# Kernel optimization log

Measured on AMD Instinct MI355X. Metric: run time of the kernel, lower is better.

The kernel has to match this reference:

```python
import jax, jax.numpy as jnp
import numpy as np

B, CIN, G, H, HW, WMIX = 128, 64, 8, 14, 16, 16  # batch, in-ch, groups, spatial, mixed width


def setup_inputs() -> dict:
    key = jax.random.key(0)
    k1, k2, k3 = jax.random.split(key, 3)
    x = jax.random.normal(k1, (B, CIN, G, H, H), dtype=jnp.float32)
    w_conv = jax.random.normal(k2, (G, 3, 3, 32), dtype=jnp.float32)   # weights[0]
    w_mix = jax.random.normal(k3, (CIN, WMIX), dtype=jnp.float32)       # weights[1]
    return {"x": x, "w_conv": w_conv, "w_mix": w_mix}


def _unfold3(t, axis, size):
    # torch F.unfold with kernel (3,1), padding (1,0) along `axis`: zero-pad by 1
    # and stack the 3 shifted windows as a new axis inserted at `axis`.
    pad = [(0, 0)] * t.ndim
    pad[axis] = (1, 1)
    p = jnp.pad(t, pad)
    slices = []
    for k in range(3):
        idx = [slice(None)] * t.ndim
        idx[axis] = slice(k, k + size)
        slices.append(p[tuple(idx)])
    return jnp.stack(slices, axis=axis)


def reference(x, w_conv, w_mix):
    # channel mix: (B, 64, 8, 14, 14) x (64, 16) -> (B, 8, 14, 14, 16)
    t4 = jnp.einsum('kjmnl,ji->kmnli', x, w_mix)
    # first unfold along H (axis 3): (B, 8, 14, 3, 14, 16)
    u1 = _unfold3(t4, 3, H)
    # second unfold along H (now axis 4): (B, 8, 14, 3, 3, 14, 16)
    u2 = _unfold3(u1, 4, H)
    # permute (0,1,2,5,4,3,6) -> (B, 8, 14, 14, 3, 3, 16)
    t5 = jnp.transpose(u2, (0, 1, 2, 5, 4, 3, 6))
    # conv channel mix: contract group(8) and both 3-taps -> (B, 14, 14, 16, 32)
    t6 = jnp.einsum('mlonikp,likj->monpj', t5, w_conv)
    # (B, 14, 14, 32, 16) -> (B, 14, 14, 512)
    t7 = jnp.transpose(t6, (0, 1, 2, 4, 3)).reshape(B, H, H, 512)
    t7 = jnp.roll(t7, 1, axis=1)  # shift_direction fixed to +1
    return jnp.transpose(t7, (0, 3, 1, 2))  # (B, 512, 14, 14)
```

## Files before the change

### kernel.cpp

```cpp
#include <hip/hip_runtime.h>

static constexpr int NB   = 128;
static constexpr int NCIN = 64;
static constexpr int NG   = 8;
static constexpr int NH   = 14;
static constexpr int NP   = 16;
static constexpr int HH   = NH * NH;
static constexpr int LROW = 20;

static constexpr int OFF_T4 = 0;
static constexpr int OFF_W2 = 2560;
static constexpr int OFF_WC = 3840;
static constexpr int OFF_XS = 2560;
static constexpr int LDS_FLOATS = 7680;

__global__ __launch_bounds__(256, 5) void fused_kernel(const float* __restrict__ x,
                                                       const float* __restrict__ wconv,
                                                       const float* __restrict__ wmix,
                                                       float* __restrict__ out) {
    __shared__ __align__(16) float lds[LDS_FLOATS];
    float*  t4s = lds + OFF_T4;
    float*  w2s = lds + OFF_W2;
    float*  wcs = lds + OFF_WC;
    float4* xs4 = reinterpret_cast<float4*>(lds + OFF_XS);

    const int tid   = threadIdx.x;
    const int b     = blockIdx.x / NH;
    const int o     = blockIdx.x % NH;
    const int o_src = (o + NH - 1) % NH;

    const float* xb = x + (size_t)b * (NCIN * NG * HH) + o_src * NH;

    const int  lane128 = tid & 127;
    const bool xact    = lane128 < 112;
    const int  jrow    = tid >> 7;
    const int  gS      = lane128 / 14;
    const int  lS      = lane128 % 14;
    const int  glst    = lane128 + (lane128 >> 3);

    float xr[16];
    const float* xb0 = xb + (size_t)(jrow * 16) * (NG * HH) + gS * HH + lS;
    if (xact) {
#pragma unroll
        for (int r = 0; r < 16; r++) xr[r] = xb0[(size_t)r * (NG * HH)];
    }

    const int gW = tid >> 5, jW = tid & 31;
    float wv9[9];
    {
        const float* wp = wconv + (size_t)(gW * 9) * 32 + jW;
#pragma unroll
        for (int t = 0; t < 9; t++) wv9[t] = wp[t * 32];
    }

#pragma unroll
    for (int r = 0; r < 3; r++) {
        int idx = r * 256 + tid;
        int gp  = idx / 6;
        int s   = idx % 6;
        int l2  = (s < 2) ? s : (14 + s);
        t4s[gp * LROW + l2] = 0.f;
    }

    if (xact) {
        float* xw = lds + OFF_XS + (jrow * 4 * 126 + glst) * 4;
#pragma unroll
        for (int r = 0; r < 16; r++)
            xw[(r >> 2) * (126 * 4) + (r & 3)] = xr[r];
    }
    __syncthreads();

    if (xact) {
        const float* xb1 = xb0 + (size_t)32 * (NG * HH);
#pragma unroll
        for (int r = 0; r < 16; r++) xr[r] = xb1[(size_t)r * (NG * HH)];
    }

    const int p0 = __builtin_amdgcn_readfirstlane((tid >> 7) << 3);
    float am[8] = {0.f, 0.f, 0.f, 0.f, 0.f, 0.f, 0.f, 0.f};

    if (xact) {
#pragma unroll
        for (int j4 = 0; j4 < 8; j4++) {
            float4 xq = xs4[j4 * 126 + glst];
#pragma unroll
            for (int pp = 0; pp < 8; pp++) {
                const int p = p0 + pp;
                am[pp] += xq.x * wmix[(j4 * 4 + 0) * NP + p]
                        + xq.y * wmix[(j4 * 4 + 1) * NP + p]
                        + xq.z * wmix[(j4 * 4 + 2) * NP + p]
                        + xq.w * wmix[(j4 * 4 + 3) * NP + p];
            }
        }
    }
    __syncthreads();
    if (xact) {
        float* xw = lds + OFF_XS + (jrow * 4 * 126 + glst) * 4;
#pragma unroll
        for (int r = 0; r < 16; r++)
            xw[(r >> 2) * (126 * 4) + (r & 3)] = xr[r];
    }
    __syncthreads();

    if (xact) {
        const float* wm1 = wmix + 32 * NP;
#pragma unroll
        for (int j4 = 0; j4 < 8; j4++) {
            float4 xq = xs4[j4 * 126 + glst];
#pragma unroll
            for (int pp = 0; pp < 8; pp++) {
                const int p = p0 + pp;
                am[pp] += xq.x * wm1[(j4 * 4 + 0) * NP + p]
                        + xq.y * wm1[(j4 * 4 + 1) * NP + p]
                        + xq.z * wm1[(j4 * 4 + 2) * NP + p]
                        + xq.w * wm1[(j4 * 4 + 3) * NP + p];
            }
        }
#pragma unroll
        for (int pp = 0; pp < 8; pp++) {
            t4s[(gS * 16 + p0 + pp) * LROW + lS + 2] = am[pp];
        }
    }
    __syncthreads();

    {
        float d0 = wv9[0];
        float d1 = wv9[1] + wv9[3];
        float d2 = wv9[2] + wv9[4] + wv9[6];
        float d3 = wv9[5] + wv9[7];
        float d4 = wv9[8];
        float* wp2 = w2s + gW * 160 + jW;
        wp2[0]   = d0;
        wp2[32]  = d1;
        wp2[64]  = d2;
        wp2[96]  = d3;
        wp2[128] = d4;
        wcs[gW * 32 + jW]       = wv9[2];
        wcs[256 + gW * 32 + jW] = wv9[6];
    }
    __syncthreads();

    const int p  = tid & 15;
    const int jh = tid >> 4;
    const int jb = jh * 2;

    float acc[NH][2];
#pragma unroll
    for (int n = 0; n < NH; n++) { acc[n][0] = 0.f; acc[n][1] = 0.f; }

    for (int g = 0; g < NG; g++) {
        float row[LROW];
        const float* rp = &t4s[(g * 16 + p) * LROW];
#pragma unroll
        for (int q = 0; q < 5; q++) {
            float4 v = *reinterpret_cast<const float4*>(rp + q * 4);
            row[q * 4 + 0] = v.x; row[q * 4 + 1] = v.y;
            row[q * 4 + 2] = v.z; row[q * 4 + 3] = v.w;
        }
#pragma unroll
        for (int di = 0; di < 5; di++) {
            float2 w = *reinterpret_cast<const float2*>(&w2s[(g * 5 + di) * 32 + jb]);
#pragma unroll
            for (int n = 0; n < NH; n++) {
                float rv = row[n + di];
                acc[n][0] += rv * w.x;
                acc[n][1] += rv * w.y;
            }
        }
        float2 c0 = *reinterpret_cast<const float2*>(&wcs[g * 32 + jb]);
        float2 c1 = *reinterpret_cast<const float2*>(&wcs[256 + g * 32 + jb]);
        float r2 = row[2], r15 = row[15];
        acc[0][0]  -= r2  * c0.x; acc[0][1]  -= r2  * c0.y;
        acc[13][0] -= r15 * c1.x; acc[13][1] -= r15 * c1.y;
    }

    __syncthreads();

    {
        int rotw = jh * 2;
        rotw -= (rotw >= 14) ? 14 : 0;
        rotw -= (rotw >= 14) ? 14 : 0;
#pragma unroll
        for (int jj = 0; jj < 2; jj++) {
            int sb = ((jb + jj) * 16 + p) * 15;
#pragma unroll
            for (int n = 0; n < NH; n++) {
                int rn = n + rotw;
                rn -= (rn >= 14) ? 14 : 0;
                lds[sb + rn] = acc[n][jj];
            }
        }
    }
    __syncthreads();

    {
        const int  k7   = tid & 7;
        const bool kact = k7 < 7;
        const int  cb   = tid >> 3;
        float* ob = out + (size_t)b * 512 * HH + (size_t)o * NH;
        if (kact) {
#pragma unroll
            for (int r = 0; r < 16; r++) {
                int c   = cb + 32 * r;
                int rot = (2 * r) % 14;
                int rn  = 2 * k7 + rot;
                rn -= (rn >= 14) ? 14 : 0;
                float v0 = lds[c * 15 + rn];
                float v1 = lds[c * 15 + rn + 1];
                *reinterpret_cast<float2*>(ob + (size_t)c * HH + 2 * k7) =
                    make_float2(v0, v1);
            }
        }
    }
}

extern "C" void kernel_launch(void* const* d_in, const int* in_sizes, int n_in,
                              void* d_out, int out_size, void* d_ws, size_t ws_size,
                              hipStream_t stream) {
    const float* x     = (const float*)d_in[0];
    const float* wconv = (const float*)d_in[1];
    const float* wmix  = (const float*)d_in[2];
    float* out = (float*)d_out;
    (void)d_ws; (void)ws_size;

    fused_kernel<<<NB * NH, 256, 0, stream>>>(x, wconv, wmix, out);
}
```

Baseline: 131.7 us.

## Drop LDS x staging, register double-buffer loads, split output transpose to cut LDS

Removes the LDS staging of x for the channel mix. Each thread now loads its 64 input channels straight from global into two 16-element register buffers, interleaving loads with FMAs. The output transpose is split into two halves so the LDS footprint shrinks (7680 to 4352 floats), and launch bounds rise to 8 blocks per CU for more occupancy. The trade-off is more register pressure, extra barriers in the store phase, and uncoalesced strided global loads replacing the shared-memory exchange.

```diff
diff --git a/kernel.cpp b/kernel.cpp
--- a/kernel.cpp
+++ b/kernel.cpp
@@ -11,39 +11,36 @@
 static constexpr int OFF_T4 = 0;
 static constexpr int OFF_W2 = 2560;
 static constexpr int OFF_WC = 3840;
-static constexpr int OFF_XS = 2560;
-static constexpr int LDS_FLOATS = 7680;
+static constexpr int LDS_FLOATS = 4352;
 
-__global__ __launch_bounds__(256, 5) void fused_kernel(const float* __restrict__ x,
+#define FMAQ(buf, qb)                                                          \
+    do {                                                                       \
+        _Pragma("unroll")                                                      \
+        for (int j4 = 0; j4 < 4; j4++) {                                       \
+            _Pragma("unroll")                                                  \
+            for (int pp = 0; pp < 8; pp++) {                                   \
+                const int p_ = p0 + pp;            \
+                am[pp] += buf[j4 * 4 + 0] * wmix[((qb) + j4 * 4 + 0) * NP + p_]\
+                        + buf[j4 * 4 + 1] * wmix[((qb) + j4 * 4 + 1) * NP + p_]\
+                        + buf[j4 * 4 + 2] * wmix[((qb) + j4 * 4 + 2) * NP + p_]\
+                        + buf[j4 * 4 + 3] * wmix[((qb) + j4 * 4 + 3) * NP + p_];\
+            }                                                                  \
+        }                                                                      \
+    } while (0)
+
+__global__ __launch_bounds__(256, 8) void fused_kernel(const float* __restrict__ x,
                                                        const float* __restrict__ wconv,
                                                        const float* __restrict__ wmix,
                                                        float* __restrict__ out) {
     __shared__ __align__(16) float lds[LDS_FLOATS];
-    float*  t4s = lds + OFF_T4;
-    float*  w2s = lds + OFF_W2;
-    float*  wcs = lds + OFF_WC;
-    float4* xs4 = reinterpret_cast<float4*>(lds + OFF_XS);
+    float* t4s = lds + OFF_T4;
+    float* w2s = lds + OFF_W2;
+    float* wcs = lds + OFF_WC;
 
     const int tid   = threadIdx.x;
     const int b     = blockIdx.x / NH;
     const int o     = blockIdx.x % NH;
     const int o_src = (o + NH - 1) % NH;
-
-    const float* xb = x + (size_t)b * (NCIN * NG * HH) + o_src * NH;
-
-    const int  lane128 = tid & 127;
-    const bool xact    = lane128 < 112;
-    const int  jrow    = tid >> 7;
-    const int  gS      = lane128 / 14;
-    const int  lS      = lane128 % 14;
-    const int  glst    = lane128 + (lane128 >> 3);
-
-    float xr[16];
-    const float* xb0 = xb + (size_t)(jrow * 16) * (NG * HH) + gS * HH + lS;
-    if (xact) {
-#pragma unroll
-        for (int r = 0; r < 16; r++) xr[r] = xb0[(size_t)r * (NG * HH)];
-    }
 
     const int gW = tid >> 5, jW = tid & 31;
     float wv9[9];
@@ -53,75 +50,19 @@
         for (int t = 0; t < 9; t++) wv9[t] = wp[t * 32];
     }
 
-#pragma unroll
-    for (int r = 0; r < 3; r++) {
-        int idx = r * 256 + tid;
-        int gp  = idx / 6;
-        int s   = idx % 6;
-        int l2  = (s < 2) ? s : (14 + s);
-        t4s[gp * LROW + l2] = 0.f;
-    }
+    const int  lane128 = tid & 127;
+    const bool xact    = lane128 < 112;
+    const int  gS      = lane128 / 14;
+    const int  lS      = lane128 % 14;
+    const int  p0      = __builtin_amdgcn_readfirstlane((tid >> 7) << 3);
+    const float* xg    = x + (size_t)b * (NCIN * NG * HH) + (size_t)gS * HH
+                           + o_src * NH + lS;
 
-    if (xact) {
-        float* xw = lds + OFF_XS + (jrow * 4 * 126 + glst) * 4;
-#pragma unroll
-        for (int r = 0; r < 16; r++)
-            xw[(r >> 2) * (126 * 4) + (r & 3)] = xr[r];
-    }
-    __syncthreads();
-
-    if (xact) {
-        const float* xb1 = xb0 + (size_t)32 * (NG * HH);
-#pragma unroll
-        for (int r = 0; r < 16; r++) xr[r] = xb1[(size_t)r * (NG * HH)];
-    }
-
-    const int p0 = __builtin_amdgcn_readfirstlane((tid >> 7) << 3);
-    float am[8] = {0.f, 0.f, 0.f, 0.f, 0.f, 0.f, 0.f, 0.f};
-
+    float xq0[16], xq1[16];
     if (xact) {
 #pragma unroll
-        for (int j4 = 0; j4 < 8; j4++) {
-            float4 xq = xs4[j4 * 126 + glst];
-#pragma unroll
-            for (int pp = 0; pp < 8; pp++) {
-                const int p = p0 + pp;
-                am[pp] += xq.x * wmix[(j4 * 4 + 0) * NP + p]
-                        + xq.y * wmix[(j4 * 4 + 1) * NP + p]
-                        + xq.z * wmix[(j4 * 4 + 2) * NP + p]
-                        + xq.w * wmix[(j4 * 4 + 3) * NP + p];
-            }
-        }
+        for (int r = 0; r < 16; r++) xq0[r] = xg[(size_t)r * (NG * HH)];
     }
-    __syncthreads();
-    if (xact) {
-        float* xw = lds + OFF_XS + (jrow * 4 * 126 + glst) * 4;
-#pragma unroll
-        for (int r = 0; r < 16; r++)
-            xw[(r >> 2) * (126 * 4) + (r & 3)] = xr[r];
-    }
-    __syncthreads();
-
-    if (xact) {
-        const float* wm1 = wmix + 32 * NP;
-#pragma unroll
-        for (int j4 = 0; j4 < 8; j4++) {
-            float4 xq = xs4[j4 * 126 + glst];
-#pragma unroll
-            for (int pp = 0; pp < 8; pp++) {
-                const int p = p0 + pp;
-                am[pp] += xq.x * wm1[(j4 * 4 + 0) * NP + p]
-                        + xq.y * wm1[(j4 * 4 + 1) * NP + p]
-                        + xq.z * wm1[(j4 * 4 + 2) * NP + p]
-                        + xq.w * wm1[(j4 * 4 + 3) * NP + p];
-            }
-        }
-#pragma unroll
-        for (int pp = 0; pp < 8; pp++) {
-            t4s[(gS * 16 + p0 + pp) * LROW + lS + 2] = am[pp];
-        }
-    }
-    __syncthreads();
 
     {
         float d0 = wv9[0];
@@ -137,6 +78,32 @@
         wp2[128] = d4;
         wcs[gW * 32 + jW]       = wv9[2];
         wcs[256 + gW * 32 + jW] = wv9[6];
+    }
+#pragma unroll
+    for (int r = 0; r < 3; r++) {
+        int idx = r * 256 + tid;
+        int gp  = idx / 6;
+        int s   = idx % 6;
+        int l2  = (s < 2) ? s : (14 + s);
+        t4s[gp * LROW + l2] = 0.f;
+    }
+
+    float am[8] = {0.f, 0.f, 0.f, 0.f, 0.f, 0.f, 0.f, 0.f};
+    if (xact) {
+#pragma unroll
+        for (int r = 0; r < 16; r++) xq1[r] = xg[(size_t)(16 + r) * (NG * HH)];
+        FMAQ(xq0, 0);
+#pragma unroll
+        for (int r = 0; r < 16; r++) xq0[r] = xg[(size_t)(32 + r) * (NG * HH)];
+        FMAQ(xq1, 16);
+#pragma unroll
+        for (int r = 0; r < 16; r++) xq1[r] = xg[(size_t)(48 + r) * (NG * HH)];
+        FMAQ(xq0, 32);
+        FMAQ(xq1, 48);
+#pragma unroll
+        for (int pp = 0; pp < 8; pp++) {
+            t4s[(gS * 16 + p0 + pp) * LROW + lS + 2] = am[pp];
+        }
     }
     __syncthreads();
 
@@ -176,41 +143,45 @@
 
     __syncthreads();
 
-    {
-        int rotw = jh * 2;
-        rotw -= (rotw >= 14) ? 14 : 0;
-        rotw -= (rotw >= 14) ? 14 : 0;
+    int rotw = jh * 2;
+    rotw -= (rotw >= 14) ? 14 : 0;
+    rotw -= (rotw >= 14) ? 14 : 0;
+
+    const int k7 = tid & 7;
+    const int cb = tid >> 3;
+    float* ob = out + (size_t)b * 512 * HH + (size_t)o * NH;
+
 #pragma unroll
-        for (int jj = 0; jj < 2; jj++) {
-            int sb = ((jb + jj) * 16 + p) * 15;
+    for (int h = 0; h < 2; h++) {
+        if ((jh >> 3) == h) {
 #pragma unroll
-            for (int n = 0; n < NH; n++) {
-                int rn = n + rotw;
-                rn -= (rn >= 14) ? 14 : 0;
-                lds[sb + rn] = acc[n][jj];
+            for (int jj = 0; jj < 2; jj++) {
+                int cl = ((jb + jj) * 16 + p) & 255;
+                int sb = cl * 15;
+#pragma unroll
+                for (int n = 0; n < NH; n++) {
+                    int rn = n + rotw;
+                    rn -= (rn >= 14) ? 14 : 0;
+                    lds[sb + rn] = acc[n][jj];
+                }
             }
         }
-    }
-    __syncthreads();
-
-    {
-        const int  k7   = tid & 7;
-        const bool kact = k7 < 7;
-        const int  cb   = tid >> 3;
-        float* ob = out + (size_t)b * 512 * HH + (size_t)o * NH;
-        if (kact) {
+        __syncthreads();
+        if (k7 < 7) {
 #pragma unroll
-            for (int r = 0; r < 16; r++) {
-                int c   = cb + 32 * r;
-                int rot = (2 * r) % 14;
+            for (int r = 0; r < 8; r++) {
+                int cl  = cb + 32 * r;
+                int cg  = h * 256 + cl;
+                int rot = (2 * (h * 8 + r)) % 14;
                 int rn  = 2 * k7 + rot;
                 rn -= (rn >= 14) ? 14 : 0;
-                float v0 = lds[c * 15 + rn];
-                float v1 = lds[c * 15 + rn + 1];
-                *reinterpret_cast<float2*>(ob + (size_t)c * HH + 2 * k7) =
+                float v0 = lds[cl * 15 + rn];
+                float v1 = lds[cl * 15 + rn + 1];
+                *reinterpret_cast<float2*>(ob + (size_t)cg * HH + 2 * k7) =
                     make_float2(v0, v1);
             }
         }
+        __syncthreads();
     }
 }
 
```

New measurement: 139.8 us. 6.1% more time.
